# Optimization experiments

Measured on AMD Instinct MI355X. Metric: run time of the kernel, lower is better.

Reference implementation:

```python
import jax, jax.numpy as jnp
import numpy as np

D_MODEL = 1024
NUM_HEADS = 16
D_K = D_MODEL // NUM_HEADS
SCALE = float(np.sqrt(D_K))


def setup_inputs() -> dict:
    key = jax.random.key(0)
    ks = jax.random.split(key, 11)
    B, S, D = 2, 2048, D_MODEL
    def lin(kw):
        # xavier-uniform-ish weight, zero bias (matches torch init style)
        lim = float(np.sqrt(6.0 / (D + D)))
        return jax.random.uniform(kw, (D, D), jnp.float32, -lim, lim)
    return {
        "q": jax.random.normal(ks[0], (B, S, D), jnp.float32),
        "k": jax.random.normal(ks[1], (B, S, D), jnp.float32),
        "v": jax.random.normal(ks[2], (B, S, D), jnp.float32),
        "Wq": lin(ks[3]), "bq": jnp.zeros((D,), jnp.float32),
        "Wk": lin(ks[4]), "bk": jnp.zeros((D,), jnp.float32),
        "Wv": lin(ks[5]), "bv": jnp.zeros((D,), jnp.float32),
        "Wo": lin(ks[6]), "bo": jnp.zeros((D,), jnp.float32),
    }


def _split_heads(x):
    B, S, _ = x.shape
    return x.reshape(B, S, NUM_HEADS, D_K).transpose(0, 2, 1, 3)  # (B,H,S,dk)


def reference(q, k, v, Wq, bq, Wk, bk, Wv, bv, Wo, bo):
    # torch nn.Linear: y = x @ W.T + b
    Q = _split_heads(q @ Wq.T + bq)
    K = _split_heads(k @ Wk.T + bk)
    V = _split_heads(v @ Wv.T + bv)
    scores = jnp.einsum("bhqd,bhkd->bhqk", Q, K) / SCALE
    # numerically-stable softmax with detached max (as in the torch code)
    m = jax.lax.stop_gradient(jnp.max(scores, axis=-1, keepdims=True))
    exp_scores = jnp.exp(scores - m)
    attn = exp_scores / (jnp.sum(exp_scores, axis=-1, keepdims=True) + 1e-9)
    out = jnp.einsum("bhqk,bhkd->bhqd", attn, V)  # (B,H,S,dk)
    B, H, S, dk = out.shape
    out = out.transpose(0, 2, 1, 3).reshape(B, S, H * dk)
    return out @ Wo.T + bo
```

## Files before the change

### kernel.cpp

```cpp
#include <hip/hip_runtime.h>


#define D_MODEL 1024
#define NHEADS  16
#define DKH     64
#define SEQ     2048
#define BATCH   2
#define MTOT    (BATCH * SEQ)
#define XE      ((long)MTOT * D_MODEL)
#define WE      ((long)D_MODEL * D_MODEL)
#define QSCALE  0.18033688011112042f

typedef __attribute__((ext_vector_type(8))) short short8v;
typedef __attribute__((ext_vector_type(4))) short short4v;
typedef __attribute__((ext_vector_type(4))) float f32x4;

typedef __attribute__((address_space(1))) void as1_void;
typedef __attribute__((address_space(3))) void as3_void;

__device__ __forceinline__ void gload16(const void* g, void* l) {
    __builtin_amdgcn_global_load_lds((const as1_void*)g, (as3_void*)l, 16, 0, 0);
}

__device__ __forceinline__ unsigned short f2bf(float x) {
    unsigned int u = __float_as_uint(x);
    u += 0x7FFFu + ((u >> 16) & 1u);
    return (unsigned short)(u >> 16);
}

__device__ __forceinline__ float fexp2(float x) {
    return __builtin_amdgcn_exp2f(x);
}

__device__ __forceinline__ unsigned int cvt_pk_bf16(float lo, float hi) {
    unsigned int r;
    asm("v_cvt_pk_bf16_f32 %0, %1, %2" : "=v"(r) : "v"(lo), "v"(hi));
    return r;
}

__device__ __forceinline__ int swz_u(int row, int col) {
    int byte = (col << 1) ^ ((row & 7) << 4);
    return (row << 6) + (byte >> 1);
}

__device__ __forceinline__ int swz_v(int d, int kv) {
    int slot = (d & 6) | ((d >> 3) & 1);
    int byte = (kv << 1) ^ (slot << 4);
    return (d << 6) + (byte >> 1);
}

struct ConvArgs {
    const float*    src[4];
    unsigned short* dst[4];
    int             n4[4];
};

__global__ __launch_bounds__(256) void convert_kernel(ConvArgs a) {
    int z = blockIdx.y;
    const float4*   s = (const float4*)a.src[z];
    unsigned short* d = a.dst[z];
    int n = a.n4[z];
    for (int i = blockIdx.x * blockDim.x + threadIdx.x; i < n;
         i += gridDim.x * blockDim.x) {
        float4 v = s[i];
        ushort4 o;
        o.x = f2bf(v.x); o.y = f2bf(v.y); o.z = f2bf(v.z); o.w = f2bf(v.w);
        *(ushort4*)(d + 4L * i) = o;
    }
}

__global__ __launch_bounds__(256) void proj_kernel(
    const float* __restrict__ xq, const float* __restrict__ xk,
    const float* __restrict__ xv, const unsigned short* __restrict__ wb,
    const float* __restrict__ bq, const float* __restrict__ bk,
    const float* __restrict__ bv, unsigned short* __restrict__ qkv) {
    __shared__ unsigned short As[2 * 128 * 32];
    __shared__ unsigned short Bs[2 * 128 * 32];

    const int t    = threadIdx.x;
    const int lane = t & 63;
    const int w    = t >> 6;
    const int wm   = w >> 1, wn = w & 1;
    const int l15  = lane & 15, g = lane >> 4;

    const int bid = blockIdx.x;
    const int xcd = bid & 7;
    const int k   = bid >> 3;
    const int ty  = (xcd << 2) | (k & 3);
    const int tx  = (k >> 2) & 7;
    const int z   = k >> 5;
    const float* bias = (z == 0) ? bq : (z == 1) ? bk : bv;
    const float scale = (z == 0) ? QSCALE : 1.0f;

    const float* Af = (z == 0) ? xq : (z == 1) ? xk : xv;
    const unsigned short* Bm = wb + (long)z * WE;
    unsigned short*       C  = qkv + (long)z * XE;
    const long m0 = (long)ty * 128;
    const long n0 = (long)tx * 128;
    const int  K  = D_MODEL;

    f32x4 acc[4][4] = {};

    const int idx0 = t, idx1 = t + 256;
    const int r0 = idx0 >> 2, c0 = (idx0 & 3) * 8;
    const int r1 = idx1 >> 2, c1 = (idx1 & 3) * 8;

    float4 a0_[2], a1_[2];

#define PLOAD_A(k0)                                                        \
    {                                                                      \
        const float* s0 = Af + (m0 + r0) * K + (k0) + c0;                  \
        const float* s1 = Af + (m0 + r1) * K + (k0) + c1;                  \
        a0_[0] = *(const float4*)(s0);                                     \
        a1_[0] = *(const float4*)(s0 + 4);                                 \
        a0_[1] = *(const float4*)(s1);                                     \
        a1_[1] = *(const float4*)(s1 + 4);                                 \
    }

#define PSTAGE_B(k0, buf)                                                  \
    gload16(Bm + (n0 + r0) * K + (k0) + c0, &Bs[(buf) * 4096 + idx0 * 8]); \
    gload16(Bm + (n0 + r1) * K + (k0) + c1, &Bs[(buf) * 4096 + idx1 * 8]);

#define PWRITE_A(buf)                                                      \
    {                                                                      \
        uint4 pk;                                                          \
        pk.x = cvt_pk_bf16(a0_[0].x, a0_[0].y);                            \
        pk.y = cvt_pk_bf16(a0_[0].z, a0_[0].w);                            \
        pk.z = cvt_pk_bf16(a1_[0].x, a1_[0].y);                            \
        pk.w = cvt_pk_bf16(a1_[0].z, a1_[0].w);                            \
        *(uint4*)&As[(buf) * 4096 + idx0 * 8] = pk;                        \
        pk.x = cvt_pk_bf16(a0_[1].x, a0_[1].y);                            \
        pk.y = cvt_pk_bf16(a0_[1].z, a0_[1].w);                            \
        pk.z = cvt_pk_bf16(a1_[1].x, a1_[1].y);                            \
        pk.w = cvt_pk_bf16(a1_[1].z, a1_[1].w);                            \
        *(uint4*)&As[(buf) * 4096 + idx1 * 8] = pk;                        \
    }

    PLOAD_A(0);
    PSTAGE_B(0, 0);
    PWRITE_A(0);
    int cur = 0;

    for (int it = 0; it < K / 32; ++it) {
        const int nxt = cur ^ 1;
        const int kn  = ((it + 1) * 32) & (K - 1);
        PLOAD_A(kn);
        PSTAGE_B(kn, nxt);
        asm volatile("s_waitcnt vmcnt(6)" ::: "memory");
        asm volatile("s_waitcnt lgkmcnt(0)" ::: "memory");
        __builtin_amdgcn_sched_barrier(0);
        __builtin_amdgcn_s_barrier();
        __builtin_amdgcn_sched_barrier(0);

        const unsigned short* Ab = &As[cur * 4096];
        const unsigned short* Bb = &Bs[cur * 4096];

        short8v af[4], bf_[4];
#pragma unroll
        for (int mf = 0; mf < 4; ++mf)
            af[mf] = *(const short8v*)&Ab[(wm * 64 + mf * 16 + l15) * 32 + g * 8];
#pragma unroll
        for (int nf = 0; nf < 4; ++nf)
            bf_[nf] = *(const short8v*)&Bb[(wn * 64 + nf * 16 + l15) * 32 + g * 8];
        __builtin_amdgcn_s_setprio(1);
#pragma unroll
        for (int mf = 0; mf < 4; ++mf)
#pragma unroll
            for (int nf = 0; nf < 4; ++nf)
                acc[mf][nf] = __builtin_amdgcn_mfma_f32_16x16x32_bf16(
                    af[mf], bf_[nf], acc[mf][nf], 0, 0, 0);
        __builtin_amdgcn_s_setprio(0);

        asm volatile("s_waitcnt lgkmcnt(0)" ::: "memory");
        __builtin_amdgcn_sched_barrier(0);
        __builtin_amdgcn_s_barrier();
        __builtin_amdgcn_sched_barrier(0);

        PWRITE_A(nxt);
        cur = nxt;
    }

    float bvv[4];
#pragma unroll
    for (int nf = 0; nf < 4; ++nf)
        bvv[nf] = bias[n0 + wn * 64 + nf * 16 + l15];

#pragma unroll
    for (int mf = 0; mf < 4; ++mf)
#pragma unroll
        for (int nf = 0; nf < 4; ++nf)
#pragma unroll
            for (int r = 0; r < 4; ++r) {
                long row = m0 + wm * 64 + mf * 16 + g * 4 + r;
                long col = n0 + wn * 64 + nf * 16 + l15;
                C[row * (long)D_MODEL + col] =
                    f2bf((acc[mf][nf][r] + bvv[nf]) * scale);
            }
#undef PLOAD_A
#undef PSTAGE_B
#undef PWRITE_A
}

__global__ __launch_bounds__(256) void out_kernel(
    const unsigned short* __restrict__ ob, const unsigned short* __restrict__ wo,
    const float* __restrict__ bo, float* __restrict__ out) {
    __shared__ unsigned short As[128 * 32];
    __shared__ unsigned short Bs[128 * 32];

    const int t    = threadIdx.x;
    const int lane = t & 63;
    const int w    = t >> 6;
    const int wm   = w >> 1, wn = w & 1;
    const int l15  = lane & 15, g = lane >> 4;

    const int bid = blockIdx.x;
    const int xcd = bid & 7;
    const int k   = bid >> 3;
    const long m0 = (long)((xcd << 2) | (k & 3)) * 128;
    const long n0 = (long)(k >> 2) * 128;
    const int  K  = D_MODEL, N = D_MODEL;

    f32x4 acc[4][4] = {};

    const int idx0 = t, idx1 = t + 256;
    const int r0 = idx0 >> 2, c0 = (idx0 & 3) * 8;
    const int r1 = idx1 >> 2, c1 = (idx1 & 3) * 8;
    const unsigned short* pa0 = ob + (m0 + r0) * K + c0;
    const unsigned short* pa1 = ob + (m0 + r1) * K + c1;
    const unsigned short* pb0 = wo + (n0 + r0) * K + c0;
    const unsigned short* pb1 = wo + (n0 + r1) * K + c1;

    for (int k0 = 0; k0 < K; k0 += 32) {
        gload16(pa0 + k0, &As[idx0 * 8]);
        gload16(pa1 + k0, &As[idx1 * 8]);
        gload16(pb0 + k0, &Bs[idx0 * 8]);
        gload16(pb1 + k0, &Bs[idx1 * 8]);
        __syncthreads();

        short8v af[4], bf_[4];
#pragma unroll
        for (int mf = 0; mf < 4; ++mf)
            af[mf] = *(const short8v*)&As[(wm * 64 + mf * 16 + l15) * 32 + g * 8];
#pragma unroll
        for (int nf = 0; nf < 4; ++nf)
            bf_[nf] = *(const short8v*)&Bs[(wn * 64 + nf * 16 + l15) * 32 + g * 8];
#pragma unroll
        for (int mf = 0; mf < 4; ++mf)
#pragma unroll
            for (int nf = 0; nf < 4; ++nf)
                acc[mf][nf] = __builtin_amdgcn_mfma_f32_16x16x32_bf16(
                    af[mf], bf_[nf], acc[mf][nf], 0, 0, 0);
        __syncthreads();
    }

    float bvv[4];
#pragma unroll
    for (int nf = 0; nf < 4; ++nf)
        bvv[nf] = bo[n0 + wn * 64 + nf * 16 + l15];

#pragma unroll
    for (int mf = 0; mf < 4; ++mf)
#pragma unroll
        for (int nf = 0; nf < 4; ++nf)
#pragma unroll
            for (int r = 0; r < 4; ++r) {
                long row = m0 + wm * 64 + mf * 16 + g * 4 + r;
                long col = n0 + wn * 64 + nf * 16 + l15;
                out[row * (long)N + col] = acc[mf][nf][r] + bvv[nf];
            }
}

#define KVB 4096

__global__ __launch_bounds__(512) void attn_kernel(
    const unsigned short* __restrict__ Qb, const unsigned short* __restrict__ Kb,
    const unsigned short* __restrict__ Vb, unsigned short* __restrict__ Ob) {
    __shared__ alignas(16) unsigned short Ks[2 * KVB];
    __shared__ alignas(16) unsigned short Vt[2 * KVB];
    __shared__ alignas(16) unsigned short Ps[8][16 * 64];
    __shared__ alignas(16) float corrS[8][16];

    const int t = threadIdx.x, lane = t & 63, w = t >> 6;
    const int l15 = lane & 15, g = lane >> 4;
    const int bid = blockIdx.x;
    const int xcd = bid & 7;
    const int kk2 = bid >> 3;
    const int bh  = (xcd << 2) | (kk2 & 3);
    const int qb  = kk2 >> 2;
    const long headoff = (long)(bh >> 4) * SEQ * D_MODEL + (long)(bh & 15) * DKH;
    const int q0w = qb * 128 + w * 16;

    short8v qf[2];
#pragma unroll
    for (int ks = 0; ks < 2; ++ks)
        qf[ks] = *(const short8v*)(Qb + headoff +
            (long)(q0w + l15) * D_MODEL + ks * 32 + g * 8);

    short8v onesv;
#pragma unroll
    for (int j = 0; j < 8; ++j) onesv[j] = (short)0x3F80;

    f32x4 o[4] = {};
    f32x4 ol = {};
    float mrun = -3.0e38f;

    const int vd0  = (t & 31) * 2;
    const int vkv0 = (t >> 5) * 4;
    const int kr0 = t >> 3, ks0 = t & 7;

    unsigned int va[4];

#define ISSUE_V(kt)                                                        \
    _Pragma("unroll")                                                      \
    for (int j = 0; j < 4; ++j)                                            \
        va[j] = *(const unsigned int*)(Vb + headoff +                      \
            (long)((kt) + vkv0 + j) * D_MODEL + vd0);

#define ISSUE_K(kt, off)                                                   \
    gload16(Kb + headoff + (long)((kt) + kr0) * D_MODEL +                  \
                ((ks0 ^ (kr0 & 7)) << 3), &Ks[(off) + t * 8]);

#define WRITE_V(off)                                                       \
    {                                                                      \
        short4v ra, rb;                                                    \
        _Pragma("unroll")                                                  \
        for (int j = 0; j < 4; ++j) {                                      \
            ra[j] = (short)(va[j] & 0xffffu);                              \
            rb[j] = (short)(va[j] >> 16);                                  \
        }                                                                  \
        *(short4v*)&Vt[(off) + swz_v(vd0,     vkv0)] = ra;                 \
        *(short4v*)&Vt[(off) + swz_v(vd0 + 1, vkv0)] = rb;                 \
    }

    asm volatile("s_waitcnt vmcnt(0)" ::: "memory");
    ISSUE_V(0);
    ISSUE_K(0, 0);
    WRITE_V(0);
    int cur = 0;

    for (int it = 0; it < SEQ / 64; ++it) {
        const int nxt = cur ^ 1;
        const int ktn = (((it + 1) & (SEQ / 64 - 1))) * 64;
        ISSUE_V(ktn);
        ISSUE_K(ktn, nxt * KVB);
        asm volatile("s_waitcnt vmcnt(5)" ::: "memory");
        asm volatile("s_waitcnt lgkmcnt(0)" ::: "memory");
        __builtin_amdgcn_sched_barrier(0);
        __builtin_amdgcn_s_barrier();
        __builtin_amdgcn_sched_barrier(0);

        const int kO = cur * KVB;

        f32x4 st[4] = {};
        __builtin_amdgcn_s_setprio(1);
#pragma unroll
        for (int ks = 0; ks < 2; ++ks)
#pragma unroll
            for (int mf = 0; mf < 4; ++mf) {
                short8v kf = *(const short8v*)&Ks[kO + swz_u(mf * 16 + l15, ks * 32 + g * 8)];
                st[mf] = __builtin_amdgcn_mfma_f32_16x16x32_bf16(
                    kf, qf[ks], st[mf], 0, 0, 0);
            }
        __builtin_amdgcn_s_setprio(0);

        float vmax = st[0][0];
#pragma unroll
        for (int mf = 0; mf < 4; ++mf)
#pragma unroll
            for (int r = 0; r < 4; ++r)
                vmax = fmaxf(vmax, st[mf][r]);
        vmax = fmaxf(vmax, __shfl_xor(vmax, 16));
        vmax = fmaxf(vmax, __shfl_xor(vmax, 32));

        const bool grow = __any(vmax > mrun + 8.0f);
        if (grow) {
            float mnew = fmaxf(mrun, vmax);
            float corr = fexp2(mrun - mnew);
            mrun = mnew;
            if (g == 0) corrS[w][l15] = corr;
        }

#pragma unroll
        for (int mf = 0; mf < 4; ++mf)
#pragma unroll
            for (int r = 0; r < 4; ++r)
                st[mf][r] = fexp2(st[mf][r] - mrun);

        unsigned short* Pw = Ps[w];
#pragma unroll
        for (int mf = 0; mf < 4; ++mf) {
            uint2 pk;
            pk.x = cvt_pk_bf16(st[mf][0], st[mf][1]);
            pk.y = cvt_pk_bf16(st[mf][2], st[mf][3]);
            *(uint2*)&Pw[swz_u(l15, mf * 16 + g * 4)] = pk;
        }

        if (grow) {
            float4 cv = *(const float4*)&corrS[w][g * 4];
#pragma unroll
            for (int nd = 0; nd < 4; ++nd)
#pragma unroll
                for (int r = 0; r < 4; ++r)
                    o[nd][r] *= cv[r];
#pragma unroll
            for (int r = 0; r < 4; ++r) ol[r] *= cv[r];
        }

        __builtin_amdgcn_s_setprio(1);
#pragma unroll
        for (int ks2 = 0; ks2 < 2; ++ks2) {
            short8v pf = *(const short8v*)&Pw[swz_u(l15, ks2 * 32 + g * 8)];
            ol = __builtin_amdgcn_mfma_f32_16x16x32_bf16(
                pf, onesv, ol, 0, 0, 0);
#pragma unroll
            for (int nd = 0; nd < 4; ++nd) {
                short8v vf = *(const short8v*)&Vt[kO + swz_v(nd * 16 + l15, ks2 * 32 + g * 8)];
                o[nd] = __builtin_amdgcn_mfma_f32_16x16x32_bf16(
                    pf, vf, o[nd], 0, 0, 0);
            }
        }
        __builtin_amdgcn_s_setprio(0);

        WRITE_V(nxt * KVB);
        cur = nxt;
    }

#pragma unroll
    for (int r = 0; r < 4; ++r) {
        float inv = 1.f / (ol[r] + 1e-9f);
        long rowoff = headoff + (long)(q0w + g * 4 + r) * D_MODEL;
#pragma unroll
        for (int nd = 0; nd < 4; ++nd)
            Ob[rowoff + nd * 16 + l15] = f2bf(o[nd][r] * inv);
    }
#undef ISSUE_V
#undef ISSUE_K
#undef WRITE_V
}

extern "C" void kernel_launch(void* const* d_in, const int* in_sizes, int n_in,
                              void* d_out, int out_size, void* d_ws, size_t ws_size,
                              hipStream_t stream) {
    unsigned short* ws  = (unsigned short*)d_ws;
    unsigned short* wb  = ws;
    unsigned short* qkv = ws + 4L * WE;
    unsigned short* ob  = qkv + 3L * XE;

    ConvArgs ca;
    ca.src[0] = (const float*)d_in[3]; ca.dst[0] = wb;           ca.n4[0] = (int)(WE / 4);
    ca.src[1] = (const float*)d_in[5]; ca.dst[1] = wb + WE;      ca.n4[1] = (int)(WE / 4);
    ca.src[2] = (const float*)d_in[7]; ca.dst[2] = wb + 2L * WE; ca.n4[2] = (int)(WE / 4);
    ca.src[3] = (const float*)d_in[9]; ca.dst[3] = wb + 3L * WE; ca.n4[3] = (int)(WE / 4);

    hipLaunchKernelGGL(convert_kernel, dim3(512, 4), dim3(256), 0, stream, ca);

    hipLaunchKernelGGL(proj_kernel, dim3(768), dim3(256), 0, stream,
                       (const float*)d_in[0], (const float*)d_in[1],
                       (const float*)d_in[2], wb,
                       (const float*)d_in[4], (const float*)d_in[6],
                       (const float*)d_in[8], qkv);

    hipLaunchKernelGGL(attn_kernel, dim3(512), dim3(512), 0, stream,
                       qkv, qkv + XE, qkv + 2L * XE, ob);

    hipLaunchKernelGGL(out_kernel, dim3(256), dim3(256), 0, stream,
                       ob, wb + 3L * WE, (const float*)d_in[10], (float*)d_out);
}
```

Before: 127.7 us.

## Fuse weight fp32-to-bf16 conversion into projection and output GEMM loads

Removes the separate weight conversion kernel and has the projection and output GEMMs load fp32 weights directly, converting them to bf16 in registers before the LDS write. The output GEMM also gains double-buffered LDS with register prefetch of the next tile in place of its single-buffered synchronous loop. This drops one launch and one write-then-read round trip of the weights. In exchange, each GEMM tile block re-reads fp32 weights, doubling weight bytes per tile, and does more conversion work in the loop.

```diff
diff --git a/kernel.cpp b/kernel.cpp
--- a/kernel.cpp
+++ b/kernel.cpp
@@ -49,29 +49,10 @@
     return (d << 6) + (byte >> 1);
 }
 
-struct ConvArgs {
-    const float*    src[4];
-    unsigned short* dst[4];
-    int             n4[4];
-};
-
-__global__ __launch_bounds__(256) void convert_kernel(ConvArgs a) {
-    int z = blockIdx.y;
-    const float4*   s = (const float4*)a.src[z];
-    unsigned short* d = a.dst[z];
-    int n = a.n4[z];
-    for (int i = blockIdx.x * blockDim.x + threadIdx.x; i < n;
-         i += gridDim.x * blockDim.x) {
-        float4 v = s[i];
-        ushort4 o;
-        o.x = f2bf(v.x); o.y = f2bf(v.y); o.z = f2bf(v.z); o.w = f2bf(v.w);
-        *(ushort4*)(d + 4L * i) = o;
-    }
-}
-
 __global__ __launch_bounds__(256) void proj_kernel(
     const float* __restrict__ xq, const float* __restrict__ xk,
-    const float* __restrict__ xv, const unsigned short* __restrict__ wb,
+    const float* __restrict__ xv, const float* __restrict__ wq,
+    const float* __restrict__ wk, const float* __restrict__ wv,
     const float* __restrict__ bq, const float* __restrict__ bk,
     const float* __restrict__ bv, unsigned short* __restrict__ qkv) {
     __shared__ unsigned short As[2 * 128 * 32];
@@ -93,8 +74,8 @@
     const float scale = (z == 0) ? QSCALE : 1.0f;
 
     const float* Af = (z == 0) ? xq : (z == 1) ? xk : xv;
-    const unsigned short* Bm = wb + (long)z * WE;
-    unsigned short*       C  = qkv + (long)z * XE;
+    const float* Wf = (z == 0) ? wq : (z == 1) ? wk : wv;
+    unsigned short* C = qkv + (long)z * XE;
     const long m0 = (long)ty * 128;
     const long n0 = (long)tx * 128;
     const int  K  = D_MODEL;
@@ -106,6 +87,7 @@
     const int r1 = idx1 >> 2, c1 = (idx1 & 3) * 8;
 
     float4 a0_[2], a1_[2];
+    float4 b0_[2], b1_[2];
 
 #define PLOAD_A(k0)                                                        \
     {                                                                      \
@@ -117,36 +99,42 @@
         a1_[1] = *(const float4*)(s1 + 4);                                 \
     }
 
-#define PSTAGE_B(k0, buf)                                                  \
-    gload16(Bm + (n0 + r0) * K + (k0) + c0, &Bs[(buf) * 4096 + idx0 * 8]); \
-    gload16(Bm + (n0 + r1) * K + (k0) + c1, &Bs[(buf) * 4096 + idx1 * 8]);
-
-#define PWRITE_A(buf)                                                      \
+#define PLOAD_B(k0)                                                        \
+    {                                                                      \
+        const float* s0 = Wf + (n0 + r0) * K + (k0) + c0;                  \
+        const float* s1 = Wf + (n0 + r1) * K + (k0) + c1;                  \
+        b0_[0] = *(const float4*)(s0);                                     \
+        b1_[0] = *(const float4*)(s0 + 4);                                 \
+        b0_[1] = *(const float4*)(s1);                                     \
+        b1_[1] = *(const float4*)(s1 + 4);                                 \
+    }
+
+#define CVT16(dst, lo, hi)                                                 \
     {                                                                      \
         uint4 pk;                                                          \
-        pk.x = cvt_pk_bf16(a0_[0].x, a0_[0].y);                            \
-        pk.y = cvt_pk_bf16(a0_[0].z, a0_[0].w);                            \
-        pk.z = cvt_pk_bf16(a1_[0].x, a1_[0].y);                            \
-        pk.w = cvt_pk_bf16(a1_[0].z, a1_[0].w);                            \
-        *(uint4*)&As[(buf) * 4096 + idx0 * 8] = pk;                        \
-        pk.x = cvt_pk_bf16(a0_[1].x, a0_[1].y);                            \
-        pk.y = cvt_pk_bf16(a0_[1].z, a0_[1].w);                            \
-        pk.z = cvt_pk_bf16(a1_[1].x, a1_[1].y);                            \
-        pk.w = cvt_pk_bf16(a1_[1].z, a1_[1].w);                            \
-        *(uint4*)&As[(buf) * 4096 + idx1 * 8] = pk;                        \
-    }
+        pk.x = cvt_pk_bf16((lo).x, (lo).y);                                \
+        pk.y = cvt_pk_bf16((lo).z, (lo).w);                                \
+        pk.z = cvt_pk_bf16((hi).x, (hi).y);                                \
+        pk.w = cvt_pk_bf16((hi).z, (hi).w);                                \
+        *(uint4*)(dst) = pk;                                               \
+    }
+
+#define PWRITE_AB(buf)                                                     \
+    CVT16(&As[(buf) * 4096 + idx0 * 8], a0_[0], a1_[0]);                   \
+    CVT16(&As[(buf) * 4096 + idx1 * 8], a0_[1], a1_[1]);                   \
+    CVT16(&Bs[(buf) * 4096 + idx0 * 8], b0_[0], b1_[0]);                   \
+    CVT16(&Bs[(buf) * 4096 + idx1 * 8], b0_[1], b1_[1]);
 
     PLOAD_A(0);
-    PSTAGE_B(0, 0);
-    PWRITE_A(0);
+    PLOAD_B(0);
+    PWRITE_AB(0);
     int cur = 0;
 
     for (int it = 0; it < K / 32; ++it) {
         const int nxt = cur ^ 1;
         const int kn  = ((it + 1) * 32) & (K - 1);
         PLOAD_A(kn);
-        PSTAGE_B(kn, nxt);
-        asm volatile("s_waitcnt vmcnt(6)" ::: "memory");
+        PLOAD_B(kn);
         asm volatile("s_waitcnt lgkmcnt(0)" ::: "memory");
         __builtin_amdgcn_sched_barrier(0);
         __builtin_amdgcn_s_barrier();
@@ -176,7 +164,7 @@
         __builtin_amdgcn_s_barrier();
         __builtin_amdgcn_sched_barrier(0);
 
-        PWRITE_A(nxt);
+        PWRITE_AB(nxt);
         cur = nxt;
     }
 
@@ -197,15 +185,15 @@
                     f2bf((acc[mf][nf][r] + bvv[nf]) * scale);
             }
 #undef PLOAD_A
-#undef PSTAGE_B
-#undef PWRITE_A
+#undef PLOAD_B
+#undef PWRITE_AB
 }
 
 __global__ __launch_bounds__(256) void out_kernel(
-    const unsigned short* __restrict__ ob, const unsigned short* __restrict__ wo,
+    const unsigned short* __restrict__ ob, const float* __restrict__ wo,
     const float* __restrict__ bo, float* __restrict__ out) {
-    __shared__ unsigned short As[128 * 32];
-    __shared__ unsigned short Bs[128 * 32];
+    __shared__ unsigned short As[2 * 128 * 32];
+    __shared__ unsigned short Bs[2 * 128 * 32];
 
     const int t    = threadIdx.x;
     const int lane = t & 63;
@@ -225,32 +213,79 @@
     const int idx0 = t, idx1 = t + 256;
     const int r0 = idx0 >> 2, c0 = (idx0 & 3) * 8;
     const int r1 = idx1 >> 2, c1 = (idx1 & 3) * 8;
-    const unsigned short* pa0 = ob + (m0 + r0) * K + c0;
-    const unsigned short* pa1 = ob + (m0 + r1) * K + c1;
-    const unsigned short* pb0 = wo + (n0 + r0) * K + c0;
-    const unsigned short* pb1 = wo + (n0 + r1) * K + c1;
-
-    for (int k0 = 0; k0 < K; k0 += 32) {
-        gload16(pa0 + k0, &As[idx0 * 8]);
-        gload16(pa1 + k0, &As[idx1 * 8]);
-        gload16(pb0 + k0, &Bs[idx0 * 8]);
-        gload16(pb1 + k0, &Bs[idx1 * 8]);
-        __syncthreads();
+
+    float4 b0_[2], b1_[2];
+
+#define OLOAD_B(k0)                                                        \
+    {                                                                      \
+        const float* s0 = wo + (n0 + r0) * K + (k0) + c0;                  \
+        const float* s1 = wo + (n0 + r1) * K + (k0) + c1;                  \
+        b0_[0] = *(const float4*)(s0);                                     \
+        b1_[0] = *(const float4*)(s0 + 4);                                 \
+        b0_[1] = *(const float4*)(s1);                                     \
+        b1_[1] = *(const float4*)(s1 + 4);                                 \
+    }
+
+#define OSTAGE_A(k0, buf)                                                  \
+    gload16(ob + (m0 + r0) * K + (k0) + c0, &As[(buf) * 4096 + idx0 * 8]); \
+    gload16(ob + (m0 + r1) * K + (k0) + c1, &As[(buf) * 4096 + idx1 * 8]);
+
+#define OCVT16(dst, lo, hi)                                                \
+    {                                                                      \
+        uint4 pk;                                                          \
+        pk.x = cvt_pk_bf16((lo).x, (lo).y);                                \
+        pk.y = cvt_pk_bf16((lo).z, (lo).w);                                \
+        pk.z = cvt_pk_bf16((hi).x, (hi).y);                                \
+        pk.w = cvt_pk_bf16((hi).z, (hi).w);                                \
+        *(uint4*)(dst) = pk;                                               \
+    }
+
+#define OWRITE_B(buf)                                                      \
+    OCVT16(&Bs[(buf) * 4096 + idx0 * 8], b0_[0], b1_[0]);                  \
+    OCVT16(&Bs[(buf) * 4096 + idx1 * 8], b0_[1], b1_[1]);
+
+    OLOAD_B(0);
+    OSTAGE_A(0, 0);
+    OWRITE_B(0);
+    int cur = 0;
+
+    for (int it = 0; it < K / 32; ++it) {
+        const int nxt = cur ^ 1;
+        const int kn  = ((it + 1) * 32) & (K - 1);
+        OLOAD_B(kn);
+        OSTAGE_A(kn, nxt);
+        asm volatile("s_waitcnt vmcnt(6)" ::: "memory");
+        asm volatile("s_waitcnt lgkmcnt(0)" ::: "memory");
+        __builtin_amdgcn_sched_barrier(0);
+        __builtin_amdgcn_s_barrier();
+        __builtin_amdgcn_sched_barrier(0);
+
+        const unsigned short* Ab = &As[cur * 4096];
+        const unsigned short* Bb = &Bs[cur * 4096];
 
         short8v af[4], bf_[4];
 #pragma unroll
         for (int mf = 0; mf < 4; ++mf)
-            af[mf] = *(const short8v*)&As[(wm * 64 + mf * 16 + l15) * 32 + g * 8];
+            af[mf] = *(const short8v*)&Ab[(wm * 64 + mf * 16 + l15) * 32 + g * 8];
 #pragma unroll
         for (int nf = 0; nf < 4; ++nf)
-            bf_[nf] = *(const short8v*)&Bs[(wn * 64 + nf * 16 + l15) * 32 + g * 8];
+            bf_[nf] = *(const short8v*)&Bb[(wn * 64 + nf * 16 + l15) * 32 + g * 8];
+        __builtin_amdgcn_s_setprio(1);
 #pragma unroll
         for (int mf = 0; mf < 4; ++mf)
 #pragma unroll
             for (int nf = 0; nf < 4; ++nf)
                 acc[mf][nf] = __builtin_amdgcn_mfma_f32_16x16x32_bf16(
                     af[mf], bf_[nf], acc[mf][nf], 0, 0, 0);
-        __syncthreads();
+        __builtin_amdgcn_s_setprio(0);
+
+        asm volatile("s_waitcnt lgkmcnt(0)" ::: "memory");
+        __builtin_amdgcn_sched_barrier(0);
+        __builtin_amdgcn_s_barrier();
+        __builtin_amdgcn_sched_barrier(0);
+
+        OWRITE_B(nxt);
+        cur = nxt;
     }
 
     float bvv[4];
@@ -268,6 +303,10 @@
                 long col = n0 + wn * 64 + nf * 16 + l15;
                 out[row * (long)N + col] = acc[mf][nf][r] + bvv[nf];
             }
+#undef OLOAD_B
+#undef OSTAGE_A
+#undef OCVT16
+#undef OWRITE_B
 }
 
 #define KVB 4096
@@ -442,21 +481,13 @@
                               void* d_out, int out_size, void* d_ws, size_t ws_size,
                               hipStream_t stream) {
     unsigned short* ws  = (unsigned short*)d_ws;
-    unsigned short* wb  = ws;
-    unsigned short* qkv = ws + 4L * WE;
+    unsigned short* qkv = ws;
     unsigned short* ob  = qkv + 3L * XE;
-
-    ConvArgs ca;
-    ca.src[0] = (const float*)d_in[3]; ca.dst[0] = wb;           ca.n4[0] = (int)(WE / 4);
-    ca.src[1] = (const float*)d_in[5]; ca.dst[1] = wb + WE;      ca.n4[1] = (int)(WE / 4);
-    ca.src[2] = (const float*)d_in[7]; ca.dst[2] = wb + 2L * WE; ca.n4[2] = (int)(WE / 4);
-    ca.src[3] = (const float*)d_in[9]; ca.dst[3] = wb + 3L * WE; ca.n4[3] = (int)(WE / 4);
-
-    hipLaunchKernelGGL(convert_kernel, dim3(512, 4), dim3(256), 0, stream, ca);
 
     hipLaunchKernelGGL(proj_kernel, dim3(768), dim3(256), 0, stream,
                        (const float*)d_in[0], (const float*)d_in[1],
-                       (const float*)d_in[2], wb,
+                       (const float*)d_in[2], (const float*)d_in[3],
+                       (const float*)d_in[5], (const float*)d_in[7],
                        (const float*)d_in[4], (const float*)d_in[6],
                        (const float*)d_in[8], qkv);
 
@@ -464,5 +495,6 @@
                        qkv, qkv + XE, qkv + 2L * XE, ob);
 
     hipLaunchKernelGGL(out_kernel, dim3(256), dim3(256), 0, stream,
-                       ob, wb + 3L * WE, (const float*)d_in[10], (float*)d_out);
-}
+                       ob, (const float*)d_in[9], (const float*)d_in[10],
+                       (float*)d_out);
+}
```

Result: slower. 135.2 us (+5.9%).
